# Kernel tuning notes

Hardware: AMD Instinct MI355X
Metric: run time of the kernel (lower is better)

Reference implementation:

```python
import jax, jax.numpy as jnp
import numpy as np

N, E, D, R = 8192, 131072, 128, 32
SIZES = (3, 5, 7)  # per-degree component counts (2l+1)
LN_EPS = 1e-5


def setup_inputs() -> dict:
    key = jax.random.key(0)
    ks = jax.random.split(key, 20)
    rn = lambda k, shape, s=1.0: jax.random.normal(k, shape, jnp.float32) * s
    inp = {
        'X0': rn(ks[0], (N, SIZES[0], D)),
        'X1': rn(ks[1], (N, SIZES[1], D)),
        'X2': rn(ks[2], (N, SIZES[2], D)),
        't_ij': rn(ks[3], (E, D)),
        'r0': rn(ks[4], (E, SIZES[0])),
        'r1': rn(ks[5], (E, SIZES[1])),
        'r2': rn(ks[6], (E, SIZES[2])),
        'edge_index': jax.random.randint(ks[7], (2, E), 0, N, dtype=jnp.int32),
        # params
        'W_vq': rn(ks[8], (D, R), D ** -0.5),
        'W_vk0': rn(ks[9], (D, R), D ** -0.5),
        'W_vk1': rn(ks[10], (D, R), D ** -0.5),
        'W_vk2': rn(ks[11], (D, R), D ** -0.5),
        'ln_g': jnp.ones((R,), jnp.float32),
        'ln_b': jnp.zeros((R,), jnp.float32),
        'W_w': rn(ks[12], (R, D), R ** -0.5),
        'b_w': jnp.zeros((D,), jnp.float32),
        'W_t1': rn(ks[13], (D, D), D ** -0.5),
        'b_t1': jnp.zeros((D,), jnp.float32),
        'W_t2': rn(ks[14], (D, D), D ** -0.5),
        'b_t2': jnp.zeros((D,), jnp.float32),
    }
    return inp


def _vec_rej(x, r):
    # x: [E, L, R], r: [E, L]; dot over component dim (L), keepdim, subtract projection
    r = r[..., None]
    dot = jnp.sum(x * r, axis=1, keepdims=True)  # [E, 1, R]
    return x - dot * r


def reference(X0, X1, X2, t_ij, r0, r1, r2, edge_index,
              W_vq, W_vk0, W_vk1, W_vk2, ln_g, ln_b, W_w, b_w,
              W_t1, b_t1, W_t2, b_t2):
    n_j, n_i = edge_index[0], edge_index[1]
    X_ls = jnp.concatenate([X0, X1, X2], axis=1)                 # [N, 15, D]
    eq_i = jnp.einsum('nld,dr->nlr', X_ls, W_vq)[n_i]            # [E, 15, R]
    ek = jnp.concatenate([
        jnp.einsum('nld,dr->nlr', X0, W_vk0),
        jnp.einsum('nld,dr->nlr', X1, W_vk1),
        jnp.einsum('nld,dr->nlr', X2, W_vk2)], axis=1)
    ek_j = ek[n_j]                                               # [E, 15, R]
    # per-degree vector rejection (vec_rej=True)
    qs, ksl, off = [], [], 0
    for r in (r0, r1, r2):
        s = r.shape[1]
        qs.append(_vec_rej(eq_i[:, off:off + s], r))
        ksl.append(_vec_rej(ek_j[:, off:off + s], -r))
        off += s
    eq_i = jnp.concatenate(qs, axis=1)
    ek_j = jnp.concatenate(ksl, axis=1)
    w_ij = jnp.sum(eq_i * ek_j, axis=1)                          # [E, R]
    # mlp_w = LayerNorm + Linear
    mu = jnp.mean(w_ij, axis=-1, keepdims=True)
    var = jnp.var(w_ij, axis=-1, keepdims=True)
    wn = (w_ij - mu) * jax.lax.rsqrt(var + LN_EPS) * ln_g + ln_b
    dw = wn @ W_w + b_w                                          # [E, D]
    # mlp_t = Linear -> silu -> Linear, then outer activation
    t = jax.nn.silu(t_ij @ W_t1 + b_t1) @ W_t2 + b_t2            # [E, D]
    return dw * jax.nn.silu(t)
```

## Files before the change

### kernel.cpp

```cpp
#include <hip/hip_runtime.h>
#include <hip/hip_bf16.h>

#define N_NODES 8192
#define N_EDGES 131072
#define LN_EPS  1e-5f

typedef __attribute__((ext_vector_type(8))) short bf16x8;
typedef __attribute__((ext_vector_type(4))) short bf16x4;
typedef __attribute__((ext_vector_type(4))) float f32x4;

__device__ __forceinline__ float silu_f(float x) {
    return x * __builtin_amdgcn_rcpf(1.0f + __expf(-x));
}

__device__ __forceinline__ unsigned short f2bf(float x) {
    union { float f; unsigned int u; } v; v.f = x;
    unsigned int r = v.u + 0x7FFFu + ((v.u >> 16) & 1u);
    return (unsigned short)(r >> 16);
}
__device__ __forceinline__ float bf2f(unsigned short u) {
    union { float f; unsigned int x; } v; v.x = ((unsigned int)u) << 16;
    return v.f;
}
__device__ __forceinline__ unsigned int pk2(float a, float b) {
    float2 t; t.x = a; t.y = b;
    union { __hip_bfloat162 h; unsigned int u; } v;
    v.h = __float22bfloat162_rn(t);
    return v.u;
}
__device__ __forceinline__ bf16x8 pack8(float4 u, float4 v) {
    union { bf16x8 b; unsigned int w[4]; } o;
    o.w[0] = pk2(u.x, u.y); o.w[1] = pk2(u.z, u.w);
    o.w[2] = pk2(v.x, v.y); o.w[3] = pk2(v.z, v.w);
    return o.b;
}
__device__ __forceinline__ bf16x4 pack4(float a, float b, float c, float d) {
    union { bf16x4 v; unsigned int u[2]; } o;
    o.u[0] = pk2(a, b); o.u[1] = pk2(c, d);
    return o.v;
}
__device__ __forceinline__ f32x4 mfma16(bf16x8 a, bf16x8 b, f32x4 c) {
    return __builtin_amdgcn_mfma_f32_16x16x32_bf16(a, b, c, 0, 0, 0);
}
#if __has_builtin(__builtin_amdgcn_mfma_f32_16x16x16bf16_1k)
__device__ __forceinline__ f32x4 mfma_k16(bf16x4 a, bf16x4 b, f32x4 c) {
    return __builtin_amdgcn_mfma_f32_16x16x16bf16_1k(a, b, c, 0, 0, 0);
}
#else
__device__ __forceinline__ f32x4 mfma_k16(bf16x4 a, bf16x4 b, f32x4 c) {
    f32x4 d;
    asm("v_mfma_f32_16x16x16_bf16 %0, %1, %2, %3"
        : "=v"(d) : "v"(a), "v"(b), "v"(c));
    return d;
}
#endif

__global__ __launch_bounds__(256) void prep_kernel(
    const float* __restrict__ W_w, const float* __restrict__ W_t1,
    const float* __restrict__ W_t2, const float* __restrict__ Wvq,
    const float* __restrict__ Wvk0, const float* __restrict__ Wvk1,
    const float* __restrict__ Wvk2,
    unsigned short* __restrict__ Wtw, unsigned short* __restrict__ Wt1b,
    unsigned short* __restrict__ Wt2b, unsigned short* __restrict__ Wqt,
    unsigned short* __restrict__ Wk0t, unsigned short* __restrict__ Wk1t,
    unsigned short* __restrict__ Wk2t)
{
    int i = blockIdx.x * 256 + threadIdx.x;
    if (i < 16384) {
        int n = i >> 7, k = i & 127;
        Wt1b[i] = f2bf(W_t1[k * 128 + n]);
        Wt2b[i] = f2bf(W_t2[k * 128 + n]);
    }
    if (i < 4096) {
        { int n = i >> 5, k = i & 31; Wtw[i] = f2bf(W_w[k * 128 + n]); }
        int r = i >> 7, d = i & 127;
        Wqt[i]  = f2bf(Wvq [d * 32 + r]);
        Wk0t[i] = f2bf(Wvk0[d * 32 + r]);
        Wk1t[i] = f2bf(Wvk1[d * 32 + r]);
        Wk2t[i] = f2bf(Wvk2[d * 32 + r]);
    }
}

template<int S, int LOFF>
__device__ __forceinline__ void proj_body(
    const float* __restrict__ X, const unsigned short* __restrict__ Wqt,
    const unsigned short* __restrict__ Wkt,
    unsigned short* __restrict__ eq, unsigned short* __restrict__ ek,
    int row0)
{
    const int tid  = threadIdx.x;
    const int lane = tid & 63;
    const int wv   = tid >> 6;
    const int l15  = lane & 15;
    const int lk   = lane >> 4;
    const int xrow = row0 + wv * 16 + l15;

    bf16x8 xf[4];
    #pragma unroll
    for (int kt = 0; kt < 4; ++kt) {
        const float* p = X + (size_t)xrow * 128 + kt * 32 + lk * 8;
        xf[kt] = pack8(*(const float4*)p, *(const float4*)(p + 4));
    }

    f32x4 qa[2], ka[2];
    #pragma unroll
    for (int h = 0; h < 2; ++h) {
        qa[h] = (f32x4){0.f, 0.f, 0.f, 0.f};
        ka[h] = (f32x4){0.f, 0.f, 0.f, 0.f};
    }
    #pragma unroll
    for (int kt = 0; kt < 4; ++kt) {
        #pragma unroll
        for (int h = 0; h < 2; ++h) {
            bf16x8 wq = *(const bf16x8*)&Wqt[(h * 16 + l15) * 128 + kt * 32 + lk * 8];
            bf16x8 wk = *(const bf16x8*)&Wkt[(h * 16 + l15) * 128 + kt * 32 + lk * 8];
            qa[h] = mfma16(wq, xf[kt], qa[h]);
            ka[h] = mfma16(wk, xf[kt], ka[h]);
        }
    }

    const int n = xrow / S;
    const int l = xrow % S + LOFF;
    const size_t base = (size_t)n * 512 + (size_t)l * 32;
    #pragma unroll
    for (int h = 0; h < 2; ++h) {
        union { ushort4 s; unsigned int u[2]; } pq, pk_;
        pq.u[0]  = pk2(qa[h][0], qa[h][1]); pq.u[1]  = pk2(qa[h][2], qa[h][3]);
        pk_.u[0] = pk2(ka[h][0], ka[h][1]); pk_.u[1] = pk2(ka[h][2], ka[h][3]);
        *(ushort4*)&eq[base + h * 16 + lk * 4] = pq.s;
        *(ushort4*)&ek[base + h * 16 + lk * 4] = pk_.s;
    }
}

__global__ __launch_bounds__(256) void proj_kernel(
    const float* __restrict__ X0, const float* __restrict__ X1,
    const float* __restrict__ X2,
    const unsigned short* __restrict__ Wqt,
    const unsigned short* __restrict__ Wk0t,
    const unsigned short* __restrict__ Wk1t,
    const unsigned short* __restrict__ Wk2t,
    unsigned short* __restrict__ eq, unsigned short* __restrict__ ek)
{
    const int b = blockIdx.x;
    if (b < 384)
        proj_body<3, 0>(X0, Wqt, Wk0t, eq, ek, b * 64);
    else if (b < 1024)
        proj_body<5, 3>(X1, Wqt, Wk1t, eq, ek, (b - 384) * 64);
    else
        proj_body<7, 8>(X2, Wqt, Wk2t, eq, ek, (b - 1024) * 64);
}

__device__ __forceinline__ float edge_w_f(
    const float* qv, const float* kv, const float* rv)
{
    float qk = 0.f;
    #pragma unroll
    for (int l = 0; l < 15; ++l) qk = fmaf(qv[l], kv[l], qk);
    float c0 = 2.f, c1 = 2.f, c2 = 2.f;
    #pragma unroll
    for (int l = 0; l < 3; ++l)  c0 -= rv[l] * rv[l];
    #pragma unroll
    for (int l = 3; l < 8; ++l)  c1 -= rv[l] * rv[l];
    #pragma unroll
    for (int l = 8; l < 15; ++l) c2 -= rv[l] * rv[l];
    float dq0 = 0.f, dk0 = 0.f, dq1 = 0.f, dk1 = 0.f, dq2 = 0.f, dk2 = 0.f;
    #pragma unroll
    for (int l = 0; l < 3; ++l)  { dq0 = fmaf(qv[l], rv[l], dq0); dk0 = fmaf(kv[l], rv[l], dk0); }
    #pragma unroll
    for (int l = 3; l < 8; ++l)  { dq1 = fmaf(qv[l], rv[l], dq1); dk1 = fmaf(kv[l], rv[l], dk1); }
    #pragma unroll
    for (int l = 8; l < 15; ++l) { dq2 = fmaf(qv[l], rv[l], dq2); dk2 = fmaf(kv[l], rv[l], dk2); }
    return qk - dq0 * dk0 * c0 - dq1 * dk1 * c1 - dq2 * dk2 * c2;
}

__global__ __launch_bounds__(256) void wn_kernel(
    const unsigned short* __restrict__ eq, const unsigned short* __restrict__ ek,
    const float* __restrict__ r0, const float* __restrict__ r1,
    const float* __restrict__ r2, const int* __restrict__ eidx,
    const float* __restrict__ ln_g, const float* __restrict__ ln_b,
    unsigned short* __restrict__ wn)
{
    const int tid = threadIdx.x;
    const int r   = tid & 31;
    const int hw  = tid >> 5;
    const int e0  = blockIdx.x * 16 + hw * 2;
    const int e1  = e0 + 1;
    const float g  = ln_g[r];
    const float bb = ln_b[r];

    const int nj0 = eidx[e0], ni0 = eidx[N_EDGES + e0];
    const int nj1 = eidx[e1], ni1 = eidx[N_EDGES + e1];

    const unsigned short* qp0 = eq + (size_t)ni0 * 512 + r;
    const unsigned short* kp0 = ek + (size_t)nj0 * 512 + r;
    const unsigned short* qp1 = eq + (size_t)ni1 * 512 + r;
    const unsigned short* kp1 = ek + (size_t)nj1 * 512 + r;

    float qv0[15], kv0[15], qv1[15], kv1[15];
    #pragma unroll
    for (int l = 0; l < 15; ++l) {
        qv0[l] = bf2f(qp0[l * 32]);
        kv0[l] = bf2f(kp0[l * 32]);
        qv1[l] = bf2f(qp1[l * 32]);
        kv1[l] = bf2f(kp1[l * 32]);
    }

    float rva[15], rvb[15];
    #pragma unroll
    for (int c = 0; c < 3; ++c) { rva[c]     = r0[e0 * 3 + c]; rvb[c]     = r0[e1 * 3 + c]; }
    #pragma unroll
    for (int c = 0; c < 5; ++c) { rva[3 + c] = r1[e0 * 5 + c]; rvb[3 + c] = r1[e1 * 5 + c]; }
    #pragma unroll
    for (int c = 0; c < 7; ++c) { rva[8 + c] = r2[e0 * 7 + c]; rvb[8 + c] = r2[e1 * 7 + c]; }

    const float w0 = edge_w_f(qv0, kv0, rva);
    const float w1 = edge_w_f(qv1, kv1, rvb);

    float s0 = w0, s20 = w0 * w0, s1 = w1, s21 = w1 * w1;
    #pragma unroll
    for (int off = 1; off < 32; off <<= 1) {
        s0  += __shfl_xor(s0,  off); s20 += __shfl_xor(s20, off);
        s1  += __shfl_xor(s1,  off); s21 += __shfl_xor(s21, off);
    }
    const float mu0   = s0 * (1.f / 32.f);
    const float var0  = s20 * (1.f / 32.f) - mu0 * mu0;
    const float mu1   = s1 * (1.f / 32.f);
    const float var1  = s21 * (1.f / 32.f) - mu1 * mu1;
    wn[(size_t)e0 * 32 + r] = f2bf((w0 - mu0) * rsqrtf(var0 + LN_EPS) * g + bb);
    wn[(size_t)e1 * 32 + r] = f2bf((w1 - mu1) * rsqrtf(var1 + LN_EPS) * g + bb);
}

__global__ __launch_bounds__(256, 4) void edge_kernel(
    const float* __restrict__ t_ij,
    const unsigned short* __restrict__ wn,
    const unsigned short* __restrict__ Wtw, const float* __restrict__ b_w,
    const unsigned short* __restrict__ Wt1, const float* __restrict__ b_t1,
    const unsigned short* __restrict__ Wt2, const float* __restrict__ b_t2,
    float* __restrict__ out)
{
    __shared__ __align__(16) unsigned short W1l[16384];
    __shared__ __align__(16) unsigned short Wwl[4096];

    const int tid  = threadIdx.x;
    const int lane = tid & 63;
    const int wv   = tid >> 6;
    const int l15  = lane & 15;
    const int lk   = lane >> 4;
    const int tile = (blockIdx.x * 4 + wv) * 32;
    const int swz7 = (l15 & 7) << 4;
    const int swz3 = (l15 & 3) << 4;

    #pragma unroll
    for (int i = 0; i < 8; ++i) {
        const int c   = tid + i * 256;
        const int row = c >> 4, c16 = c & 15;
        const int off = (row * 256 + c16 * 16) ^ ((row & 7) << 4);
        *(uint4*)((char*)W1l + off) = *(const uint4*)&Wt1[row * 128 + c16 * 8];
    }
    #pragma unroll
    for (int i = 0; i < 2; ++i) {
        const int c   = tid + i * 256;
        const int row = c >> 2, c4 = c & 3;
        uint4 v = *(const uint4*)&Wtw[row * 32 + c4 * 8];
        *(uint4*)((char*)Wwl + ((row * 64 + c4 * 16) ^ ((row & 3) << 4))) = v;
    }

    bf16x8 a1[4][2];
    #pragma unroll
    for (int kt = 0; kt < 4; ++kt)
        #pragma unroll
        for (int rt = 0; rt < 2; ++rt) {
            const float* p = t_ij + (size_t)(tile + rt * 16 + l15) * 128
                           + kt * 32 + lk * 8;
            a1[kt][rt] = pack8(*(const float4*)p, *(const float4*)(p + 4));
        }

    bf16x8 wnf[2];
    #pragma unroll
    for (int rt = 0; rt < 2; ++rt)
        wnf[rt] = *(const bf16x8*)&wn[(size_t)(tile + rt * 16 + l15) * 32 + lk * 8];

    __syncthreads();

    bf16x4 h[2][8];
    #pragma unroll
    for (int ct = 0; ct < 8; ++ct) {
        bf16x8 w1f[4];
        #pragma unroll
        for (int kt = 0; kt < 4; ++kt)
            w1f[kt] = *(const bf16x8*)((const char*)W1l +
                (((ct * 16 + l15) * 256 + kt * 64 + lk * 16) ^ swz7));
        f32x4 ac[2];
        #pragma unroll
        for (int rt = 0; rt < 2; ++rt) ac[rt] = (f32x4){0.f, 0.f, 0.f, 0.f};
        #pragma unroll
        for (int kt = 0; kt < 4; ++kt)
            #pragma unroll
            for (int rt = 0; rt < 2; ++rt)
                ac[rt] = mfma16(w1f[kt], a1[kt][rt], ac[rt]);

        const float4 bt1 = *(const float4*)&b_t1[ct * 16 + lk * 4];
        #pragma unroll
        for (int rt = 0; rt < 2; ++rt)
            h[rt][ct] = pack4(silu_f(ac[rt][0] + bt1.x),
                              silu_f(ac[rt][1] + bt1.y),
                              silu_f(ac[rt][2] + bt1.z),
                              silu_f(ac[rt][3] + bt1.w));
    }

    #pragma unroll
    for (int ct2 = 0; ct2 < 8; ++ct2) {
        bf16x4 w2b[8];
        #pragma unroll
        for (int ct1 = 0; ct1 < 8; ++ct1)
            w2b[ct1] = *(const bf16x4*)&Wt2[(size_t)(ct2 * 16 + l15) * 128
                                            + ct1 * 16 + lk * 4];
        bf16x8 wwf = *(const bf16x8*)((const char*)Wwl +
            (((ct2 * 16 + l15) * 64 + lk * 16) ^ swz3));
        const float bwv = b_w[ct2 * 16 + l15];
        const float b2v = b_t2[ct2 * 16 + l15];

        #pragma unroll
        for (int rt = 0; rt < 2; ++rt) {
            f32x4 o = (f32x4){0.f, 0.f, 0.f, 0.f};
            #pragma unroll
            for (int ct1 = 0; ct1 < 8; ++ct1)
                o = mfma_k16(h[rt][ct1], w2b[ct1], o);
            f32x4 d = mfma16(wnf[rt], wwf, (f32x4){0.f, 0.f, 0.f, 0.f});

            float* op = out + (size_t)(tile + rt * 16 + lk * 4) * 128
                      + ct2 * 16 + l15;
            #pragma unroll
            for (int j = 0; j < 4; ++j)
                op[j * 128] = (d[j] + bwv) * silu_f(o[j] + b2v);
        }
    }
}

extern "C" void kernel_launch(void* const* d_in, const int* in_sizes, int n_in,
                              void* d_out, int out_size, void* d_ws, size_t ws_size,
                              hipStream_t stream) {
    (void)in_sizes; (void)n_in; (void)out_size; (void)ws_size;
    const float* X0   = (const float*)d_in[0];
    const float* X1   = (const float*)d_in[1];
    const float* X2   = (const float*)d_in[2];
    const float* t_ij = (const float*)d_in[3];
    const float* r0   = (const float*)d_in[4];
    const float* r1   = (const float*)d_in[5];
    const float* r2   = (const float*)d_in[6];
    const int*   eidx = (const int*)d_in[7];
    const float* Wvq  = (const float*)d_in[8];
    const float* Wvk0 = (const float*)d_in[9];
    const float* Wvk1 = (const float*)d_in[10];
    const float* Wvk2 = (const float*)d_in[11];
    const float* ln_g = (const float*)d_in[12];
    const float* ln_b = (const float*)d_in[13];
    const float* W_w  = (const float*)d_in[14];
    const float* b_w  = (const float*)d_in[15];
    const float* W_t1 = (const float*)d_in[16];
    const float* b_t1 = (const float*)d_in[17];
    const float* W_t2 = (const float*)d_in[18];
    const float* b_t2 = (const float*)d_in[19];
    float* out = (float*)d_out;

    unsigned short* eq   = (unsigned short*)d_ws;
    unsigned short* ek   = eq  + (size_t)N_NODES * 512;
    unsigned short* wn   = ek  + (size_t)N_NODES * 512;
    unsigned short* Wtw  = wn  + (size_t)N_EDGES * 32;
    unsigned short* Wt1b = Wtw  + 4096;
    unsigned short* Wt2b = Wt1b + 16384;
    unsigned short* Wqt  = Wt2b + 16384;
    unsigned short* Wk0t = Wqt  + 4096;
    unsigned short* Wk1t = Wk0t + 4096;
    unsigned short* Wk2t = Wk1t + 4096;

    prep_kernel<<<64, 256, 0, stream>>>(W_w, W_t1, W_t2, Wvq, Wvk0, Wvk1, Wvk2,
                                        Wtw, Wt1b, Wt2b, Wqt, Wk0t, Wk1t, Wk2t);
    proj_kernel<<<1920, 256, 0, stream>>>(X0, X1, X2, Wqt, Wk0t, Wk1t, Wk2t,
                                          eq, ek);
    wn_kernel<<<N_EDGES / 16, 256, 0, stream>>>(eq, ek, r0, r1, r2, eidx,
                                                ln_g, ln_b, wn);
    edge_kernel<<<N_EDGES / 128, 256, 0, stream>>>(t_ij, wn, Wtw, b_w,
                                                   Wt1b, b_t1, Wt2b, b_t2, out);
}
```

Before: 112.8 us.

## Stage W_t2 in LDS and process two edge tiles per wave in edge kernel

The edge kernel now copies W_t2 into swizzled shared memory alongside W_t1, instead of reading it from global memory per wave. Each block handles 256 edges, with every wave running two 32-edge tiles in sequence, so the weight staging cost is spread over twice as many edges and half as many blocks are launched. The launch-bounds occupancy hint is dropped and all of the second tile's inputs are prefetched up front. This raises register and LDS pressure (about 72KB of LDS per block), which may lower occupancy and latency hiding.

```diff
diff --git a/kernel.cpp b/kernel.cpp
--- a/kernel.cpp
+++ b/kernel.cpp
@@ -230,7 +230,7 @@
     wn[(size_t)e1 * 32 + r] = f2bf((w1 - mu1) * rsqrtf(var1 + LN_EPS) * g + bb);
 }
 
-__global__ __launch_bounds__(256, 4) void edge_kernel(
+__global__ __launch_bounds__(256) void edge_kernel(
     const float* __restrict__ t_ij,
     const unsigned short* __restrict__ wn,
     const unsigned short* __restrict__ Wtw, const float* __restrict__ b_w,
@@ -239,6 +239,7 @@
     float* __restrict__ out)
 {
     __shared__ __align__(16) unsigned short W1l[16384];
+    __shared__ __align__(16) unsigned short W2l[16384];
     __shared__ __align__(16) unsigned short Wwl[4096];
 
     const int tid  = threadIdx.x;
@@ -246,9 +247,10 @@
     const int wv   = tid >> 6;
     const int l15  = lane & 15;
     const int lk   = lane >> 4;
-    const int tile = (blockIdx.x * 4 + wv) * 32;
     const int swz7 = (l15 & 7) << 4;
     const int swz3 = (l15 & 3) << 4;
+    const int tile0 = blockIdx.x * 256 + wv * 32;
+    const int tile1 = tile0 + 128;
 
     #pragma unroll
     for (int i = 0; i < 8; ++i) {
@@ -256,6 +258,7 @@
         const int row = c >> 4, c16 = c & 15;
         const int off = (row * 256 + c16 * 16) ^ ((row & 7) << 4);
         *(uint4*)((char*)W1l + off) = *(const uint4*)&Wt1[row * 128 + c16 * 8];
+        *(uint4*)((char*)W2l + off) = *(const uint4*)&Wt2[row * 128 + c16 * 8];
     }
     #pragma unroll
     for (int i = 0; i < 2; ++i) {
@@ -265,76 +268,84 @@
         *(uint4*)((char*)Wwl + ((row * 64 + c4 * 16) ^ ((row & 3) << 4))) = v;
     }
 
-    bf16x8 a1[4][2];
+    bf16x8 a1a[4][2], a1b[4][2], wnfa[2], wnfb[2];
     #pragma unroll
     for (int kt = 0; kt < 4; ++kt)
         #pragma unroll
         for (int rt = 0; rt < 2; ++rt) {
-            const float* p = t_ij + (size_t)(tile + rt * 16 + l15) * 128
-                           + kt * 32 + lk * 8;
-            a1[kt][rt] = pack8(*(const float4*)p, *(const float4*)(p + 4));
+            const float* pa = t_ij + (size_t)(tile0 + rt * 16 + l15) * 128
+                            + kt * 32 + lk * 8;
+            const float* pb = t_ij + (size_t)(tile1 + rt * 16 + l15) * 128
+                            + kt * 32 + lk * 8;
+            a1a[kt][rt] = pack8(*(const float4*)pa, *(const float4*)(pa + 4));
+            a1b[kt][rt] = pack8(*(const float4*)pb, *(const float4*)(pb + 4));
         }
-
-    bf16x8 wnf[2];
-    #pragma unroll
-    for (int rt = 0; rt < 2; ++rt)
-        wnf[rt] = *(const bf16x8*)&wn[(size_t)(tile + rt * 16 + l15) * 32 + lk * 8];
+    #pragma unroll
+    for (int rt = 0; rt < 2; ++rt) {
+        wnfa[rt] = *(const bf16x8*)&wn[(size_t)(tile0 + rt * 16 + l15) * 32 + lk * 8];
+        wnfb[rt] = *(const bf16x8*)&wn[(size_t)(tile1 + rt * 16 + l15) * 32 + lk * 8];
+    }
 
     __syncthreads();
 
-    bf16x4 h[2][8];
-    #pragma unroll
-    for (int ct = 0; ct < 8; ++ct) {
-        bf16x8 w1f[4];
+    auto process = [&](int tile, bf16x8 (&a1)[4][2], bf16x8 (&wnf)[2]) {
+        bf16x4 h[2][8];
         #pragma unroll
-        for (int kt = 0; kt < 4; ++kt)
-            w1f[kt] = *(const bf16x8*)((const char*)W1l +
-                (((ct * 16 + l15) * 256 + kt * 64 + lk * 16) ^ swz7));
-        f32x4 ac[2];
+        for (int ct = 0; ct < 8; ++ct) {
+            bf16x8 w1f[4];
+            #pragma unroll
+            for (int kt = 0; kt < 4; ++kt)
+                w1f[kt] = *(const bf16x8*)((const char*)W1l +
+                    (((ct * 16 + l15) * 256 + kt * 64 + lk * 16) ^ swz7));
+            f32x4 ac[2];
+            #pragma unroll
+            for (int rt = 0; rt < 2; ++rt) ac[rt] = (f32x4){0.f, 0.f, 0.f, 0.f};
+            #pragma unroll
+            for (int kt = 0; kt < 4; ++kt)
+                #pragma unroll
+                for (int rt = 0; rt < 2; ++rt)
+                    ac[rt] = mfma16(w1f[kt], a1[kt][rt], ac[rt]);
+
+            const float4 bt1 = *(const float4*)&b_t1[ct * 16 + lk * 4];
+            #pragma unroll
+            for (int rt = 0; rt < 2; ++rt)
+                h[rt][ct] = pack4(silu_f(ac[rt][0] + bt1.x),
+                                  silu_f(ac[rt][1] + bt1.y),
+                                  silu_f(ac[rt][2] + bt1.z),
+                                  silu_f(ac[rt][3] + bt1.w));
+        }
+
         #pragma unroll
-        for (int rt = 0; rt < 2; ++rt) ac[rt] = (f32x4){0.f, 0.f, 0.f, 0.f};
-        #pragma unroll
-        for (int kt = 0; kt < 4; ++kt)
-            #pragma unroll
-            for (int rt = 0; rt < 2; ++rt)
-                ac[rt] = mfma16(w1f[kt], a1[kt][rt], ac[rt]);
-
-        const float4 bt1 = *(const float4*)&b_t1[ct * 16 + lk * 4];
-        #pragma unroll
-        for (int rt = 0; rt < 2; ++rt)
-            h[rt][ct] = pack4(silu_f(ac[rt][0] + bt1.x),
-                              silu_f(ac[rt][1] + bt1.y),
-                              silu_f(ac[rt][2] + bt1.z),
-                              silu_f(ac[rt][3] + bt1.w));
-    }
-
-    #pragma unroll
-    for (int ct2 = 0; ct2 < 8; ++ct2) {
-        bf16x4 w2b[8];
-        #pragma unroll
-        for (int ct1 = 0; ct1 < 8; ++ct1)
-            w2b[ct1] = *(const bf16x4*)&Wt2[(size_t)(ct2 * 16 + l15) * 128
-                                            + ct1 * 16 + lk * 4];
-        bf16x8 wwf = *(const bf16x8*)((const char*)Wwl +
-            (((ct2 * 16 + l15) * 64 + lk * 16) ^ swz3));
-        const float bwv = b_w[ct2 * 16 + l15];
-        const float b2v = b_t2[ct2 * 16 + l15];
-
-        #pragma unroll
-        for (int rt = 0; rt < 2; ++rt) {
-            f32x4 o = (f32x4){0.f, 0.f, 0.f, 0.f};
+        for (int ct2 = 0; ct2 < 8; ++ct2) {
+            bf16x4 w2b[8];
             #pragma unroll
             for (int ct1 = 0; ct1 < 8; ++ct1)
-                o = mfma_k16(h[rt][ct1], w2b[ct1], o);
-            f32x4 d = mfma16(wnf[rt], wwf, (f32x4){0.f, 0.f, 0.f, 0.f});
-
-            float* op = out + (size_t)(tile + rt * 16 + lk * 4) * 128
-                      + ct2 * 16 + l15;
-            #pragma unroll
-            for (int j = 0; j < 4; ++j)
-                op[j * 128] = (d[j] + bwv) * silu_f(o[j] + b2v);
+                w2b[ct1] = *(const bf16x4*)((const char*)W2l +
+                    (((ct2 * 16 + l15) * 256 + ct1 * 32 + lk * 8) ^ swz7));
+            bf16x8 wwf = *(const bf16x8*)((const char*)Wwl +
+                (((ct2 * 16 + l15) * 64 + lk * 16) ^ swz3));
+            const float bwv = b_w[ct2 * 16 + l15];
+            const float b2v = b_t2[ct2 * 16 + l15];
+
+            #pragma unroll
+            for (int rt = 0; rt < 2; ++rt) {
+                f32x4 o = (f32x4){0.f, 0.f, 0.f, 0.f};
+                #pragma unroll
+                for (int ct1 = 0; ct1 < 8; ++ct1)
+                    o = mfma_k16(h[rt][ct1], w2b[ct1], o);
+                f32x4 d = mfma16(wnf[rt], wwf, (f32x4){0.f, 0.f, 0.f, 0.f});
+
+                float* op = out + (size_t)(tile + rt * 16 + lk * 4) * 128
+                          + ct2 * 16 + l15;
+                #pragma unroll
+                for (int j = 0; j < 4; ++j)
+                    op[j * 128] = (d[j] + bwv) * silu_f(o[j] + b2v);
+            }
         }
-    }
+    };
+
+    process(tile0, a1a, wnfa);
+    process(tile1, a1b, wnfb);
 }
 
 extern "C" void kernel_launch(void* const* d_in, const int* in_sizes, int n_in,
@@ -380,6 +391,6 @@
                                           eq, ek);
     wn_kernel<<<N_EDGES / 16, 256, 0, stream>>>(eq, ek, r0, r1, r2, eidx,
                                                 ln_g, ln_b, wn);
-    edge_kernel<<<N_EDGES / 128, 256, 0, stream>>>(t_ij, wn, Wtw, b_w,
+    edge_kernel<<<N_EDGES / 256, 256, 0, stream>>>(t_ij, wn, Wtw, b_w,
                                                    Wt1b, b_t1, Wt2b, b_t2, out);
 }
```

After: 97.27 us. 1.16x faster.
